# Kernel tuning notes

Hardware: AMD Instinct MI355X
Metric: run time of the kernel (lower is better)

The kernel has to match this reference:

```python
import jax, jax.numpy as jnp
import numpy as np

WINDOW = 60
DEPTH = 3
HIDDEN = 256
LN_EPS = 1e-5


def _lyndon_indices(d):
    # Lyndon words over alphabet {0..d-1}, lengths 2 and 3, lexicographic order
    # (signatory mode='words' extracts expanded-logsig coefficients at Lyndon words).
    i2 = np.array([(i, j) for i in range(d) for j in range(d) if (i, j) < (j, i)], dtype=np.int32)
    i3 = np.array([(i, j, k) for i in range(d) for j in range(d) for k in range(d)
                   if (i, j, k) < (j, k, i) and (i, j, k) < (k, i, j)], dtype=np.int32)
    return i2, i3


def _logsig_features(x):
    # x: [b, s, c] -> logsignature of time-augmented sliding windows: [b*s, sig_channels]
    b, s, c = x.shape
    d = c + 1
    # replicate-padded sliding windows via clipped gather (matches F.pad replicate + unfold)
    pos = jnp.clip(jnp.arange(s)[:, None] + jnp.arange(WINDOW)[None, :] - (WINDOW - 1), 0, s - 1)
    windows = x[:, pos, :]                                   # [b, s, W, c]
    t = jnp.linspace(0.0, 1.0, WINDOW, dtype=x.dtype)        # time augmentation channel
    t_b = jnp.broadcast_to(t[None, None, :, None], (b, s, WINDOW, 1))
    aug = jnp.concatenate([t_b, windows], axis=-1).reshape(b * s, WINDOW, d)
    N = b * s
    # basepoint=True: prepend zero point -> increments include the first point itself
    inc = jnp.diff(aug, axis=1, prepend=jnp.zeros((N, 1, d), aug.dtype))  # [N, W, d]
    inc_t = jnp.transpose(inc, (1, 0, 2))                    # [W, N, d]

    def chen_step(carry, v):
        S1, S2, S3 = carry
        vv = jnp.einsum('ni,nj->nij', v, v)
        vvv = jnp.einsum('nij,nk->nijk', vv, v)
        nS3 = S3 + jnp.einsum('nij,nk->nijk', S2, v) \
                 + 0.5 * jnp.einsum('ni,njk->nijk', S1, vv) + vvv / 6.0
        nS2 = S2 + jnp.einsum('ni,nj->nij', S1, v) + 0.5 * vv
        nS1 = S1 + v
        return (nS1, nS2, nS3), None

    init = (jnp.zeros((N, d), x.dtype), jnp.zeros((N, d, d), x.dtype), jnp.zeros((N, d, d, d), x.dtype))
    (S1, S2, S3), _ = jax.lax.scan(chen_step, init, inc_t)
    # log in truncated tensor algebra: log(1+x) = x - x^2/2 + x^3/3
    L1 = S1
    L2 = S2 - 0.5 * jnp.einsum('ni,nj->nij', S1, S1)
    L3 = (S3 - 0.5 * (jnp.einsum('ni,njk->nijk', S1, S2) + jnp.einsum('nij,nk->nijk', S2, S1))
          + jnp.einsum('ni,nj,nk->nijk', S1, S1, S1) / 3.0)
    i2, i3 = _lyndon_indices(d)
    f2 = L2[:, i2[:, 0], i2[:, 1]]
    f3 = L3[:, i3[:, 0], i3[:, 1], i3[:, 2]]
    return jnp.concatenate([L1, f2, f3], axis=-1)            # [N, sig_channels]


def setup_inputs() -> dict:
    key = jax.random.key(0)
    ks = jax.random.split(key, 5)
    b, s, c = 8, 2048, 8
    d = c + 1
    sig_channels = d + (d * d - d) // 2 + (d ** 3 - d) // 3  # 285 for d=9
    h2 = 2 * HIDDEN
    x = jax.random.normal(ks[0], (b, s, c), dtype=jnp.float32)
    w1 = jax.random.normal(ks[1], (sig_channels, h2), dtype=jnp.float32) / np.sqrt(sig_channels)
    b1 = jnp.zeros((h2,), jnp.float32)
    ln_g = jnp.ones((h2,), jnp.float32)
    ln_b = jnp.zeros((h2,), jnp.float32)
    w2 = jax.random.normal(ks[2], (h2, HIDDEN), dtype=jnp.float32) / np.sqrt(h2)
    b2 = jnp.zeros((HIDDEN,), jnp.float32)
    return {"x": x, "w1": w1, "b1": b1, "ln_g": ln_g, "ln_b": ln_b, "w2": w2, "b2": b2}


def reference(x, w1, b1, ln_g, ln_b, w2, b2):
    b, s, _ = x.shape
    feats = _logsig_features(x)                              # [b*s, sig_channels]
    h = jax.nn.gelu(feats @ w1 + b1, approximate=False)      # torch default GELU (erf)
    mu = jnp.mean(h, axis=-1, keepdims=True)
    var = jnp.var(h, axis=-1, keepdims=True)
    h = (h - mu) / jnp.sqrt(var + LN_EPS) * ln_g + ln_b      # LayerNorm; Dropout is eval no-op
    out = h @ w2 + b2
    return out.reshape(b, s, -1)
```

## Files before the change

### kernel.cpp

```cpp
#include <hip/hip_runtime.h>
#include <hip/hip_bf16.h>
#include <cstdint>
#include <cstddef>

typedef short short8 __attribute__((ext_vector_type(8)));
typedef float f32x4 __attribute__((ext_vector_type(4)));
typedef float f32x2 __attribute__((ext_vector_type(2)));

#define NS    2048
#define KPAD  288
#define H2    512
#define HID   256
#define WPB   7
#define SBLK  293

#define MFMA(a,b,c) __builtin_amdgcn_mfma_f32_16x16x32_bf16((a),(b),(c),0,0,0)

__device__ __forceinline__ void gl2lds16(const void* g, void* l) {
    __builtin_amdgcn_global_load_lds(
        (const __attribute__((address_space(1))) void*)g,
        (__attribute__((address_space(3))) void*)l, 16, 0, 0);
}
__device__ __forceinline__ float geluf(float x) {
    return 0.5f * x * (1.0f + erff(x * 0.70710678118654752f));
}
__device__ __forceinline__ f32x4 shfl4(f32x4 v, int d) {
    f32x4 r;
    r[0] = __shfl_xor(v[0], d); r[1] = __shfl_xor(v[1], d);
    r[2] = __shfl_xor(v[2], d); r[3] = __shfl_xor(v[3], d);
    return r;
}

struct Tbl3 { short col[729]; };
static constexpr Tbl3 make_tbl3() {
    Tbl3 t{};
    for (int x = 0; x < 729; ++x) t.col[x] = -1;
    int r = 0;
    for (int i = 0; i < 9; ++i)
        for (int j = 0; j < 9; ++j)
            for (int k = 0; k < 9; ++k) {
                bool lt1 = (i < j) || (i == j && (j < k || (j == k && k < i)));
                bool lt2 = (i < k) || (i == k && (j < i || (j == i && k < j)));
                if (lt1 && lt2) { t.col[(i*9+j)*9+k] = (short)(45 + r); ++r; }
            }
    return t;
}
static constexpr Tbl3 TBL3 = make_tbl3();

#define SIG_STEP(VA_,VB_,VC_) { \
    const float hh = 0.5f * S1i + vi * (1.0f/6.0f); \
    const float ra = S2ra + hh * (VA_); \
    const float rb = S2rb + hh * (VB_); \
    const float rc = S2rc + hh * (VC_); \
    const f32x2 ra2 = {ra, ra}, rb2 = {rb, rb}, rc2 = {rc, rc}; \
    S3sa += ra * v0; S3pa0 += ra2*vp0; S3pa1 += ra2*vp1; S3pa2 += ra2*vp2; S3pa3 += ra2*vp3; \
    S3sb += rb * v0; S3pb0 += rb2*vp0; S3pb1 += rb2*vp1; S3pb2 += rb2*vp2; S3pb3 += rb2*vp3; \
    S3sc += rc * v0; S3pc0 += rc2*vp0; S3pc1 += rc2*vp1; S3pc2 += rc2*vp2; S3pc3 += rc2*vp3; \
    const float aa = S1i + 0.5f * vi; \
    S2ra += aa * (VA_); S2rb += aa * (VB_); S2rc += aa * (VC_); \
    S1i += vi; }

#define SIG_MAIN(VA_,VB_,VC_) { \
    { const float* xr = &X[(g0 - lo) * 8]; \
      const float4 e0 = *(const float4*)xr; \
      const float4 e1 = *(const float4*)(xr + 4); \
      const float rs = xr[ioff]; \
      const float v0 = 0.0f; \
      const f32x2 vp0 = {e0.x, e0.y}, vp1 = {e0.z, e0.w}, vp2 = {e1.x, e1.y}, vp3 = {e1.z, e1.w}; \
      const float vi = (ci == 0) ? 0.0f : rs; \
      SIG_STEP(VA_,VB_,VC_) } \
    const float* pd = &PD[(sm59 + 1 - lo + 59) * 8]; \
    float4 d0 = *(const float4*)pd; \
    float4 d1 = *(const float4*)(pd + 4); \
    float rn = pd[ioff]; \
    _Pragma("unroll 2") \
    for (int j = 1; j < 60; ++j) { \
      const float4 e0 = d0; const float4 e1 = d1; const float rs = rn; \
      pd += 8; \
      d0 = *(const float4*)pd; d1 = *(const float4*)(pd + 4); rn = pd[ioff]; \
      const float v0 = DT; \
      const f32x2 vp0 = {e0.x, e0.y}, vp1 = {e0.z, e0.w}, vp2 = {e1.x, e1.y}, vp3 = {e1.z, e1.w}; \
      const float vi = (ci == 0) ? DT : rs; \
      SIG_STEP(VA_,VB_,VC_) \
    } }

#define SIG_ST(RA,RB,RC) \
    if (act) { \
        if ((RA) == 0) S1buf[widx * 9 + ci] = S1i; \
        float* sb = &S2buf[widx * 81 + ci * 9]; \
        sb[RA] = S2ra; sb[RB] = S2rb; sb[RC] = S2rc; \
    }

#define S3EL0(SL) S3s##SL
#define S3EL1(SL) S3p##SL##0[0]
#define S3EL2(SL) S3p##SL##0[1]
#define S3EL3(SL) S3p##SL##1[0]
#define S3EL4(SL) S3p##SL##1[1]
#define S3EL5(SL) S3p##SL##2[0]
#define S3EL6(SL) S3p##SL##2[1]
#define S3EL7(SL) S3p##SL##3[0]
#define S3EL8(SL) S3p##SL##3[1]

#define SIG_E2(SL,J2) if (ci < (J2)) { \
    const float val2 = S2r##SL - 0.5f * S1i * s1v##J2; \
    const int col2 = 9 + ci*8 - (ci*(ci-1))/2 + ((J2) - ci - 1); \
    frow[col2] = __float2bfloat16(val2); }

#define SIG_E3(SL,R,K) { const int col3 = TBL3.col[tb + (R)*9 + (K)]; \
    if (col3 >= 0) { \
        const float val3 = S3EL##K(SL) \
            - 0.5f * (S1i * S2w[(R)*9+(K)] + S2r##SL * s1v##K) \
            + S1i * s1v##R * s1v##K * (1.0f/3.0f); \
        frow[col3] = __float2bfloat16(val3); } }

#define SIG_E3R(SL,R) SIG_E3(SL,R,0) SIG_E3(SL,R,1) SIG_E3(SL,R,2) SIG_E3(SL,R,3) \
    SIG_E3(SL,R,4) SIG_E3(SL,R,5) SIG_E3(SL,R,6) SIG_E3(SL,R,7) SIG_E3(SL,R,8)

#define SIG_EMIT(RA,RB,RC) \
    if (act) { \
        if ((RA) == 0) { \
            frow[ci] = __float2bfloat16(S1i); \
            if (ci == 0) { \
                const __hip_bfloat16 z16 = __float2bfloat16(0.0f); \
                frow[285] = z16; frow[286] = z16; frow[287] = z16; \
            } \
        } \
        SIG_E2(a,RA) SIG_E2(b,RB) SIG_E2(c,RC) \
        SIG_E3R(a,RA) SIG_E3R(b,RB) SIG_E3R(c,RC) \
    }

__global__ __launch_bounds__(192) __attribute__((amdgpu_waves_per_eu(1, 6)))
void sig_kernel(const float* __restrict__ x, __hip_bfloat16* __restrict__ feats) {
    __shared__ __align__(16) float X[66 * 8];
    __shared__ __align__(16) float PD[126 * 8];
    __shared__ float S2buf[WPB * 81];
    __shared__ float S1buf[WPB * 9];

    const int blk = blockIdx.x;
    const int b   = blk / SBLK;
    const int s0  = (blk % SBLK) * WPB;
    const int lo  = (s0 - 59 > 0) ? (s0 - 59) : 0;
    const int hi  = (s0 + WPB - 1 < NS - 1) ? (s0 + WPB - 1) : (NS - 1);
    const int nrow = hi - lo + 1;
    const int tid = threadIdx.x;

    {
        const float4* src = (const float4*)(x + ((size_t)b * NS + lo) * 8);
        float4* X4 = (float4*)X;
        const int n4 = nrow * 2;
        for (int t = tid; t < n4; t += 192) X4[t] = src[t];
    }
    __syncthreads();
    {
        const float4* X4 = (const float4*)X;
        float4* PD4 = (float4*)PD;
        for (int t = tid; t < 252; t += 192) {
            const int p = t >> 1;
            const int r = p - 59;
            float4 dv = {0.f, 0.f, 0.f, 0.f};
            if (r > 0 && r < nrow) {
                const float4 a = X4[t - 118], bb = X4[t - 120];
                dv.x = a.x - bb.x; dv.y = a.y - bb.y; dv.z = a.z - bb.z; dv.w = a.w - bb.w;
            }
            PD4[t] = dv;
        }
    }
    __syncthreads();

    const int t3    = tid >> 6;
    const int lt    = tid & 63;
    const int widx0 = lt / 9;
    const int ci    = lt - widx0 * 9;
    const bool act  = (lt < 63) && (s0 + widx0 < NS);
    const int widx  = (widx0 < WPB - 1) ? widx0 : WPB - 1;
    int s = s0 + widx; if (s > NS - 1) s = NS - 1;

    float S3sa=0.f, S3sb=0.f, S3sc=0.f;
    f32x2 S3pa0={0.f,0.f},S3pa1={0.f,0.f},S3pa2={0.f,0.f},S3pa3={0.f,0.f};
    f32x2 S3pb0={0.f,0.f},S3pb1={0.f,0.f},S3pb2={0.f,0.f},S3pb3={0.f,0.f};
    f32x2 S3pc0={0.f,0.f},S3pc1={0.f,0.f},S3pc2={0.f,0.f},S3pc3={0.f,0.f};
    float S2ra=0.f, S2rb=0.f, S2rc=0.f;
    float S1i = 0.f;
    const int ioff = (ci > 0) ? (ci - 1) : 0;
    const int sm59 = s - 59;
    const int g0   = (sm59 > 0) ? sm59 : 0;
    const float DT = 1.0f / 59.0f;

    if (t3 == 0)      { SIG_MAIN(v0,   e0.x, e0.y) }
    else if (t3 == 1) { SIG_MAIN(e0.z, e0.w, e1.x) }
    else              { SIG_MAIN(e1.y, e1.z, e1.w) }

    if (t3 == 0)      { SIG_ST(0,1,2) }
    else if (t3 == 1) { SIG_ST(3,4,5) }
    else              { SIG_ST(6,7,8) }
    __syncthreads();

    const float* s1p = &S1buf[widx * 9];
    const float s1v0=s1p[0], s1v1=s1p[1], s1v2=s1p[2], s1v3=s1p[3], s1v4=s1p[4];
    const float s1v5=s1p[5], s1v6=s1p[6], s1v7=s1p[7], s1v8=s1p[8];
    const float* S2w = &S2buf[widx * 81];
    const int tb = ci * 81;
    __hip_bfloat16* frow = feats + (size_t)(b * NS + s) * KPAD;

    if (t3 == 0)      { SIG_EMIT(0,1,2) }
    else if (t3 == 1) { SIG_EMIT(3,4,5) }
    else              { SIG_EMIT(6,7,8) }
}

__global__ __launch_bounds__(512)
void prep_kernel(const float* __restrict__ w1, const float* __restrict__ w2,
                 const float* __restrict__ lng, const float* __restrict__ lnb,
                 const float* __restrict__ b2,
                 __hip_bfloat16* __restrict__ w1T, __hip_bfloat16* __restrict__ w2g,
                 float* __restrict__ gw, float* __restrict__ cvec,
                 float* __restrict__ stats) {
    const int blk = blockIdx.x;
    if (blk < 256) {
        const int n = blk, k = threadIdx.x;
        const float wv = w2[(size_t)k * HID + n];
        const float a = lng[k] * wv;
        const float c = lnb[k] * wv;
        w2g[(size_t)n * H2 + k] = __float2bfloat16(a);
        float ra = a, rc = c;
#pragma unroll
        for (int d = 1; d < 64; d <<= 1) { ra += __shfl_xor(ra, d); rc += __shfl_xor(rc, d); }
        __shared__ float r1[8], r2[8];
        const int wv_ = k >> 6, ln = k & 63;
        if (ln == 0) { r1[wv_] = ra; r2[wv_] = rc; }
        __syncthreads();
        if (k == 0) {
            float sa = 0.f, sc = 0.f;
#pragma unroll
            for (int i = 0; i < 8; ++i) { sa += r1[i]; sc += r2[i]; }
            gw[n] = sa; cvec[n] = sc + b2[n];
        }
    } else {
        const int n = blk - 256;
        const int k = threadIdx.x;
        if (k < KPAD) {
            const float v = (k < 285) ? w1[(size_t)k * H2 + n] : 0.0f;
            w1T[(size_t)n * KPAD + k] = __float2bfloat16(v);
        }
        if (k < 64) stats[n * 64 + k] = 0.0f;
    }
}

#define GDECL \
    f32x4 acc00={0,0,0,0},acc01={0,0,0,0},acc02={0,0,0,0},acc03={0,0,0,0}; \
    f32x4 acc10={0,0,0,0},acc11={0,0,0,0},acc12={0,0,0,0},acc13={0,0,0,0}; \
    f32x4 acc20={0,0,0,0},acc21={0,0,0,0},acc22={0,0,0,0},acc23={0,0,0,0}; \
    f32x4 acc30={0,0,0,0},acc31={0,0,0,0},acc32={0,0,0,0},acc33={0,0,0,0};

#define GMROW(mf) { const short8 av = *(const short8*)(abase + (mf)*512); \
    acc##mf##0 = MFMA(av, b0v, acc##mf##0); acc##mf##1 = MFMA(av, b1v, acc##mf##1); \
    acc##mf##2 = MFMA(av, b2v, acc##mf##2); acc##mf##3 = MFMA(av, b3v, acc##mf##3); }

#define GSTAGE(APTR, BPTR, KD, K0, LA, LB) { \
    int c = tid; \
    gl2lds16((APTR) + (size_t)(m0 + (c>>2))*(KD) + (K0) + (c&3)*8, (char*)(LA) + (c & ~63)*16); \
    gl2lds16((BPTR) + (size_t)(n0 + (c>>2))*(KD) + (K0) + (c&3)*8, (char*)(LB) + (c & ~63)*16); \
    c = tid + 256; \
    gl2lds16((APTR) + (size_t)(m0 + (c>>2))*(KD) + (K0) + (c&3)*8, (char*)(LA) + (c & ~63)*16); \
    gl2lds16((BPTR) + (size_t)(n0 + (c>>2))*(KD) + (K0) + (c&3)*8, (char*)(LB) + (c & ~63)*16); }

#define GCOMP(LA, LB) { \
    const __hip_bfloat16* abase = (LA) + (mh + l16)*32 + quad*8; \
    const __hip_bfloat16* bbase = (LB) + (nh + l16)*32 + quad*8; \
    const short8 b0v = *(const short8*)(bbase); \
    const short8 b1v = *(const short8*)(bbase + 512); \
    const short8 b2v = *(const short8*)(bbase + 1024); \
    const short8 b3v = *(const short8*)(bbase + 1536); \
    GMROW(0) GMROW(1) GMROW(2) GMROW(3) }

#define GEMM_PIPE(APTR, BPTR, KD, KSTEPS) \
    GSTAGE(APTR, BPTR, KD, 0, ldsA0, ldsB0) \
    __syncthreads(); \
    _Pragma("unroll 1") \
    for (int kt = 0; kt < (KSTEPS); kt += 2) { \
        if (kt + 1 < (KSTEPS)) { GSTAGE(APTR, BPTR, KD, (kt+1)*32, ldsA1, ldsB1) } \
        GCOMP(ldsA0, ldsB0) \
        __syncthreads(); \
        if (kt + 1 < (KSTEPS)) { \
            if (kt + 2 < (KSTEPS)) { GSTAGE(APTR, BPTR, KD, (kt+2)*32, ldsA0, ldsB0) } \
            GCOMP(ldsA1, ldsB1) \
            __syncthreads(); \
        } \
    }

#define G1EP(mf,nf) { \
    const int colv = n0 + nh + (nf)*16 + l16; \
    const float bv = bias[colv]; \
    f32x4 e; \
    e[0] = geluf(acc##mf##nf[0] + bv); e[1] = geluf(acc##mf##nf[1] + bv); \
    e[2] = geluf(acc##mf##nf[2] + bv); e[3] = geluf(acc##mf##nf[3] + bv); \
    const int rrow = m0 + mh + (mf)*16 + quad*4; \
    h1[(size_t)(rrow+0)*H2 + colv] = __float2bfloat16(e[0]); \
    h1[(size_t)(rrow+1)*H2 + colv] = __float2bfloat16(e[1]); \
    h1[(size_t)(rrow+2)*H2 + colv] = __float2bfloat16(e[2]); \
    h1[(size_t)(rrow+3)*H2 + colv] = __float2bfloat16(e[3]); \
    sum##mf += e; sq##mf += e*e; }

#define G1RED(mf) { \
    f32x4 s = sum##mf, q = sq##mf; \
    s += shfl4(s,1); q += shfl4(q,1); s += shfl4(s,2); q += shfl4(q,2); \
    s += shfl4(s,4); q += shfl4(q,4); s += shfl4(s,8); q += shfl4(q,8); \
    if (l16 == 0) { const int rrow = m0 + mh + (mf)*16 + quad*4; \
        atomicAdd(&stats[2*(rrow+0)],   s[0]); atomicAdd(&stats[2*(rrow+0)+1], q[0]); \
        atomicAdd(&stats[2*(rrow+1)],   s[1]); atomicAdd(&stats[2*(rrow+1)+1], q[1]); \
        atomicAdd(&stats[2*(rrow+2)],   s[2]); atomicAdd(&stats[2*(rrow+2)+1], q[2]); \
        atomicAdd(&stats[2*(rrow+3)],   s[3]); atomicAdd(&stats[2*(rrow+3)+1], q[3]); } }

__global__ __launch_bounds__(256) __attribute__((amdgpu_waves_per_eu(1, 4)))
void gemm1_kernel(const __hip_bfloat16* __restrict__ feats,
                  const __hip_bfloat16* __restrict__ w1T,
                  const float* __restrict__ bias,
                  __hip_bfloat16* __restrict__ h1,
                  float* __restrict__ stats) {
    __shared__ __align__(16) __hip_bfloat16 ldsA0[128 * 32];
    __shared__ __align__(16) __hip_bfloat16 ldsB0[128 * 32];
    __shared__ __align__(16) __hip_bfloat16 ldsA1[128 * 32];
    __shared__ __align__(16) __hip_bfloat16 ldsB1[128 * 32];
    const int tid  = threadIdx.x;
    const int wave = tid >> 6;
    const int lane = tid & 63;
    const int quad = lane >> 4;
    const int l16  = lane & 15;
    const int mh   = (wave >> 1) * 64;
    const int nh   = (wave & 1) * 64;
    const int m0   = blockIdx.x * 128;
    const int n0   = blockIdx.y * 128;
    GDECL
    GEMM_PIPE(feats, w1T, KPAD, 9)
    f32x4 sum0={0,0,0,0},sum1={0,0,0,0},sum2={0,0,0,0},sum3={0,0,0,0};
    f32x4 sq0={0,0,0,0},sq1={0,0,0,0},sq2={0,0,0,0},sq3={0,0,0,0};
    G1EP(0,0) G1EP(0,1) G1EP(0,2) G1EP(0,3)
    G1EP(1,0) G1EP(1,1) G1EP(1,2) G1EP(1,3)
    G1EP(2,0) G1EP(2,1) G1EP(2,2) G1EP(2,3)
    G1EP(3,0) G1EP(3,1) G1EP(3,2) G1EP(3,3)
    G1RED(0) G1RED(1) G1RED(2) G1RED(3)
}

#define STATR(r) { const float su = stats[2*(rrow+(r))]; const float qu = stats[2*(rrow+(r))+1]; \
    const float m_ = su * (1.0f/512.0f); const float v_ = qu * (1.0f/512.0f) - m_*m_; \
    muv[r] = m_; rsv[r] = rsqrtf(v_ + 1e-5f); }

#define G2C(mf,nf) { const int colv = n0 + nh + (nf)*16 + l16; \
    const float g_ = gw[colv], c_ = cvec[colv]; \
    out[(size_t)(rrow+0)*HID + colv] = rsv[0]*(acc##mf##nf[0] - muv[0]*g_) + c_; \
    out[(size_t)(rrow+1)*HID + colv] = rsv[1]*(acc##mf##nf[1] - muv[1]*g_) + c_; \
    out[(size_t)(rrow+2)*HID + colv] = rsv[2]*(acc##mf##nf[2] - muv[2]*g_) + c_; \
    out[(size_t)(rrow+3)*HID + colv] = rsv[3]*(acc##mf##nf[3] - muv[3]*g_) + c_; }

#define G2EP(mf) { const int rrow = m0 + mh + (mf)*16 + quad*4; \
    f32x4 muv, rsv; \
    STATR(0) STATR(1) STATR(2) STATR(3) \
    G2C(mf,0) G2C(mf,1) G2C(mf,2) G2C(mf,3) }

__global__ __launch_bounds__(256) __attribute__((amdgpu_waves_per_eu(1, 4)))
void gemm2_kernel(const __hip_bfloat16* __restrict__ h1,
                  const __hip_bfloat16* __restrict__ w2g,
                  const float* __restrict__ stats,
                  const float* __restrict__ gw,
                  const float* __restrict__ cvec,
                  float* __restrict__ out) {
    __shared__ __align__(16) __hip_bfloat16 ldsA0[128 * 32];
    __shared__ __align__(16) __hip_bfloat16 ldsB0[128 * 32];
    __shared__ __align__(16) __hip_bfloat16 ldsA1[128 * 32];
    __shared__ __align__(16) __hip_bfloat16 ldsB1[128 * 32];
    const int tid  = threadIdx.x;
    const int wave = tid >> 6;
    const int lane = tid & 63;
    const int quad = lane >> 4;
    const int l16  = lane & 15;
    const int mh   = (wave >> 1) * 64;
    const int nh   = (wave & 1) * 64;
    const int m0   = blockIdx.x * 128;
    const int n0   = blockIdx.y * 128;
    GDECL
    GEMM_PIPE(h1, w2g, H2, 16)
    G2EP(0) G2EP(1) G2EP(2) G2EP(3)
}

extern "C" void kernel_launch(void* const* d_in, const int* in_sizes, int n_in,
                              void* d_out, int out_size, void* d_ws, size_t ws_size,
                              hipStream_t stream) {
    const float* x   = (const float*)d_in[0];
    const float* w1  = (const float*)d_in[1];
    const float* b1  = (const float*)d_in[2];
    const float* lng = (const float*)d_in[3];
    const float* lnb = (const float*)d_in[4];
    const float* w2  = (const float*)d_in[5];
    const float* b2  = (const float*)d_in[6];
    float* out = (float*)d_out;

    char* ws = (char*)d_ws;
    __hip_bfloat16* feats = (__hip_bfloat16*)(ws);
    __hip_bfloat16* h1    = (__hip_bfloat16*)(ws + 9437184);
    __hip_bfloat16* w1T   = (__hip_bfloat16*)(ws + 26214400);
    __hip_bfloat16* w2g   = (__hip_bfloat16*)(ws + 26509312);
    float*          gw    = (float*)(ws + 26771456);
    float*          cvec  = (float*)(ws + 26775552);
    float*          stats = (float*)(ws + 26779648);

    prep_kernel<<<dim3(768), dim3(512), 0, stream>>>(w1, w2, lng, lnb, b2,
                                                     w1T, w2g, gw, cvec, stats);
    sig_kernel<<<dim3(8 * SBLK), dim3(192), 0, stream>>>(x, feats);
    gemm1_kernel<<<dim3(128, 4), dim3(256), 0, stream>>>(feats, w1T, b1, h1, stats);
    gemm2_kernel<<<dim3(128, 2), dim3(256), 0, stream>>>(h1, w2g, stats, gw, cvec, out);
}
```

Baseline: 155.5 us.

## Fuse both MLP GEMMs and LayerNorm into one kernel keeping hidden activations in LDS

Replaces the separate gemm1 and gemm2 kernels with a single mlp_kernel in which each block owns 32 rows. GEMM1 computes all 512 hidden columns per row, applies GELU, and writes the bf16 result into a swizzled LDS buffer. LayerNorm row statistics are reduced in shared memory instead of through global atomics. GEMM2 then reads the hidden tile straight from LDS. This removes the h1 round trip through global memory, one kernel launch, and the atomic stats buffer, but every block now streams the full W1 and W2 weights with a small 32-row M tile and uses a large LDS footprint, which limits occupancy.

```diff
diff --git a/kernel.cpp b/kernel.cpp
--- a/kernel.cpp
+++ b/kernel.cpp
@@ -212,8 +212,7 @@
                  const float* __restrict__ lng, const float* __restrict__ lnb,
                  const float* __restrict__ b2,
                  __hip_bfloat16* __restrict__ w1T, __hip_bfloat16* __restrict__ w2g,
-                 float* __restrict__ gw, float* __restrict__ cvec,
-                 float* __restrict__ stats) {
+                 float* __restrict__ gw, float* __restrict__ cvec) {
     const int blk = blockIdx.x;
     if (blk < 256) {
         const int n = blk, k = threadIdx.x;
@@ -241,144 +240,165 @@
             const float v = (k < 285) ? w1[(size_t)k * H2 + n] : 0.0f;
             w1T[(size_t)n * KPAD + k] = __float2bfloat16(v);
         }
-        if (k < 64) stats[n * 64 + k] = 0.0f;
-    }
-}
-
-#define GDECL \
-    f32x4 acc00={0,0,0,0},acc01={0,0,0,0},acc02={0,0,0,0},acc03={0,0,0,0}; \
-    f32x4 acc10={0,0,0,0},acc11={0,0,0,0},acc12={0,0,0,0},acc13={0,0,0,0}; \
-    f32x4 acc20={0,0,0,0},acc21={0,0,0,0},acc22={0,0,0,0},acc23={0,0,0,0}; \
-    f32x4 acc30={0,0,0,0},acc31={0,0,0,0},acc32={0,0,0,0},acc33={0,0,0,0};
-
-#define GMROW(mf) { const short8 av = *(const short8*)(abase + (mf)*512); \
-    acc##mf##0 = MFMA(av, b0v, acc##mf##0); acc##mf##1 = MFMA(av, b1v, acc##mf##1); \
-    acc##mf##2 = MFMA(av, b2v, acc##mf##2); acc##mf##3 = MFMA(av, b3v, acc##mf##3); }
-
-#define GSTAGE(APTR, BPTR, KD, K0, LA, LB) { \
-    int c = tid; \
-    gl2lds16((APTR) + (size_t)(m0 + (c>>2))*(KD) + (K0) + (c&3)*8, (char*)(LA) + (c & ~63)*16); \
-    gl2lds16((BPTR) + (size_t)(n0 + (c>>2))*(KD) + (K0) + (c&3)*8, (char*)(LB) + (c & ~63)*16); \
-    c = tid + 256; \
-    gl2lds16((APTR) + (size_t)(m0 + (c>>2))*(KD) + (K0) + (c&3)*8, (char*)(LA) + (c & ~63)*16); \
-    gl2lds16((BPTR) + (size_t)(n0 + (c>>2))*(KD) + (K0) + (c&3)*8, (char*)(LB) + (c & ~63)*16); }
-
-#define GCOMP(LA, LB) { \
-    const __hip_bfloat16* abase = (LA) + (mh + l16)*32 + quad*8; \
-    const __hip_bfloat16* bbase = (LB) + (nh + l16)*32 + quad*8; \
-    const short8 b0v = *(const short8*)(bbase); \
-    const short8 b1v = *(const short8*)(bbase + 512); \
-    const short8 b2v = *(const short8*)(bbase + 1024); \
-    const short8 b3v = *(const short8*)(bbase + 1536); \
-    GMROW(0) GMROW(1) GMROW(2) GMROW(3) }
-
-#define GEMM_PIPE(APTR, BPTR, KD, KSTEPS) \
-    GSTAGE(APTR, BPTR, KD, 0, ldsA0, ldsB0) \
-    __syncthreads(); \
-    _Pragma("unroll 1") \
-    for (int kt = 0; kt < (KSTEPS); kt += 2) { \
-        if (kt + 1 < (KSTEPS)) { GSTAGE(APTR, BPTR, KD, (kt+1)*32, ldsA1, ldsB1) } \
-        GCOMP(ldsA0, ldsB0) \
-        __syncthreads(); \
-        if (kt + 1 < (KSTEPS)) { \
-            if (kt + 2 < (KSTEPS)) { GSTAGE(APTR, BPTR, KD, (kt+2)*32, ldsA0, ldsB0) } \
-            GCOMP(ldsA1, ldsB1) \
-            __syncthreads(); \
-        } \
-    }
-
-#define G1EP(mf,nf) { \
-    const int colv = n0 + nh + (nf)*16 + l16; \
-    const float bv = bias[colv]; \
-    f32x4 e; \
-    e[0] = geluf(acc##mf##nf[0] + bv); e[1] = geluf(acc##mf##nf[1] + bv); \
-    e[2] = geluf(acc##mf##nf[2] + bv); e[3] = geluf(acc##mf##nf[3] + bv); \
-    const int rrow = m0 + mh + (mf)*16 + quad*4; \
-    h1[(size_t)(rrow+0)*H2 + colv] = __float2bfloat16(e[0]); \
-    h1[(size_t)(rrow+1)*H2 + colv] = __float2bfloat16(e[1]); \
-    h1[(size_t)(rrow+2)*H2 + colv] = __float2bfloat16(e[2]); \
-    h1[(size_t)(rrow+3)*H2 + colv] = __float2bfloat16(e[3]); \
-    sum##mf += e; sq##mf += e*e; }
-
-#define G1RED(mf) { \
-    f32x4 s = sum##mf, q = sq##mf; \
-    s += shfl4(s,1); q += shfl4(q,1); s += shfl4(s,2); q += shfl4(q,2); \
-    s += shfl4(s,4); q += shfl4(q,4); s += shfl4(s,8); q += shfl4(q,8); \
-    if (l16 == 0) { const int rrow = m0 + mh + (mf)*16 + quad*4; \
-        atomicAdd(&stats[2*(rrow+0)],   s[0]); atomicAdd(&stats[2*(rrow+0)+1], q[0]); \
-        atomicAdd(&stats[2*(rrow+1)],   s[1]); atomicAdd(&stats[2*(rrow+1)+1], q[1]); \
-        atomicAdd(&stats[2*(rrow+2)],   s[2]); atomicAdd(&stats[2*(rrow+2)+1], q[2]); \
-        atomicAdd(&stats[2*(rrow+3)],   s[3]); atomicAdd(&stats[2*(rrow+3)+1], q[3]); } }
-
-__global__ __launch_bounds__(256) __attribute__((amdgpu_waves_per_eu(1, 4)))
-void gemm1_kernel(const __hip_bfloat16* __restrict__ feats,
-                  const __hip_bfloat16* __restrict__ w1T,
-                  const float* __restrict__ bias,
-                  __hip_bfloat16* __restrict__ h1,
-                  float* __restrict__ stats) {
-    __shared__ __align__(16) __hip_bfloat16 ldsA0[128 * 32];
-    __shared__ __align__(16) __hip_bfloat16 ldsB0[128 * 32];
-    __shared__ __align__(16) __hip_bfloat16 ldsA1[128 * 32];
-    __shared__ __align__(16) __hip_bfloat16 ldsB1[128 * 32];
+    }
+}
+
+__global__ __launch_bounds__(256)
+void mlp_kernel(const __hip_bfloat16* __restrict__ feats,
+                const __hip_bfloat16* __restrict__ w1T,
+                const float* __restrict__ bias,
+                const __hip_bfloat16* __restrict__ w2g,
+                const float* __restrict__ gw,
+                const float* __restrict__ cvec,
+                float* __restrict__ out) {
+    __shared__ __align__(16) __hip_bfloat16 Blds[512 * 32];
+    __shared__ __align__(16) __hip_bfloat16 Hbuf[32 * 512];
+    __shared__ __align__(16) __hip_bfloat16 Ab0[32 * 32];
+    __shared__ __align__(16) __hip_bfloat16 Ab1[32 * 32];
+    __shared__ float sstat[4][32][2];
+
     const int tid  = threadIdx.x;
     const int wave = tid >> 6;
     const int lane = tid & 63;
     const int quad = lane >> 4;
     const int l16  = lane & 15;
-    const int mh   = (wave >> 1) * 64;
-    const int nh   = (wave & 1) * 64;
-    const int m0   = blockIdx.x * 128;
-    const int n0   = blockIdx.y * 128;
-    GDECL
-    GEMM_PIPE(feats, w1T, KPAD, 9)
-    f32x4 sum0={0,0,0,0},sum1={0,0,0,0},sum2={0,0,0,0},sum3={0,0,0,0};
-    f32x4 sq0={0,0,0,0},sq1={0,0,0,0},sq2={0,0,0,0},sq3={0,0,0,0};
-    G1EP(0,0) G1EP(0,1) G1EP(0,2) G1EP(0,3)
-    G1EP(1,0) G1EP(1,1) G1EP(1,2) G1EP(1,3)
-    G1EP(2,0) G1EP(2,1) G1EP(2,2) G1EP(2,3)
-    G1EP(3,0) G1EP(3,1) G1EP(3,2) G1EP(3,3)
-    G1RED(0) G1RED(1) G1RED(2) G1RED(3)
-}
-
-#define STATR(r) { const float su = stats[2*(rrow+(r))]; const float qu = stats[2*(rrow+(r))+1]; \
-    const float m_ = su * (1.0f/512.0f); const float v_ = qu * (1.0f/512.0f) - m_*m_; \
-    muv[r] = m_; rsv[r] = rsqrtf(v_ + 1e-5f); }
-
-#define G2C(mf,nf) { const int colv = n0 + nh + (nf)*16 + l16; \
-    const float g_ = gw[colv], c_ = cvec[colv]; \
-    out[(size_t)(rrow+0)*HID + colv] = rsv[0]*(acc##mf##nf[0] - muv[0]*g_) + c_; \
-    out[(size_t)(rrow+1)*HID + colv] = rsv[1]*(acc##mf##nf[1] - muv[1]*g_) + c_; \
-    out[(size_t)(rrow+2)*HID + colv] = rsv[2]*(acc##mf##nf[2] - muv[2]*g_) + c_; \
-    out[(size_t)(rrow+3)*HID + colv] = rsv[3]*(acc##mf##nf[3] - muv[3]*g_) + c_; }
-
-#define G2EP(mf) { const int rrow = m0 + mh + (mf)*16 + quad*4; \
-    f32x4 muv, rsv; \
-    STATR(0) STATR(1) STATR(2) STATR(3) \
-    G2C(mf,0) G2C(mf,1) G2C(mf,2) G2C(mf,3) }
-
-__global__ __launch_bounds__(256) __attribute__((amdgpu_waves_per_eu(1, 4)))
-void gemm2_kernel(const __hip_bfloat16* __restrict__ h1,
-                  const __hip_bfloat16* __restrict__ w2g,
-                  const float* __restrict__ stats,
-                  const float* __restrict__ gw,
-                  const float* __restrict__ cvec,
-                  float* __restrict__ out) {
-    __shared__ __align__(16) __hip_bfloat16 ldsA0[128 * 32];
-    __shared__ __align__(16) __hip_bfloat16 ldsB0[128 * 32];
-    __shared__ __align__(16) __hip_bfloat16 ldsA1[128 * 32];
-    __shared__ __align__(16) __hip_bfloat16 ldsB1[128 * 32];
-    const int tid  = threadIdx.x;
-    const int wave = tid >> 6;
-    const int lane = tid & 63;
-    const int quad = lane >> 4;
-    const int l16  = lane & 15;
-    const int mh   = (wave >> 1) * 64;
-    const int nh   = (wave & 1) * 64;
-    const int m0   = blockIdx.x * 128;
-    const int n0   = blockIdx.y * 128;
-    GDECL
-    GEMM_PIPE(h1, w2g, H2, 16)
-    G2EP(0) G2EP(1) G2EP(2) G2EP(3)
+    const int m0   = blockIdx.x * 32;
+    const int swz16 = (quad ^ ((l16 >> 1) & 3)) * 16;
+
+#define STAGE_B1(S, DST) { \
+    _Pragma("unroll") \
+    for (int i_ = 0; i_ < 8; ++i_) { \
+        const int c_ = tid + i_ * 256; const int r_ = c_ >> 2; const int q_ = c_ & 3; \
+        gl2lds16(w1T + (size_t)r_ * KPAD + (S) * 32 + ((q_ ^ ((r_ >> 1) & 3)) * 8), \
+                 (char*)(DST) + (c_ & ~63) * 16); } }
+#define STAGE_A(S, DST) { if (tid < 128) { \
+        const int r_ = tid >> 2; const int q_ = tid & 3; \
+        gl2lds16(feats + (size_t)(m0 + r_) * KPAD + (S) * 32 + ((q_ ^ ((r_ >> 1) & 3)) * 8), \
+                 (char*)(DST) + (tid & ~63) * 16); } }
+#define STAGE_B2(T, DST) { \
+    _Pragma("unroll") \
+    for (int i_ = 0; i_ < 4; ++i_) { \
+        const int c_ = tid + i_ * 256; const int r_ = c_ >> 2; const int q_ = c_ & 3; \
+        gl2lds16(w2g + (size_t)r_ * H2 + (T) * 32 + ((q_ ^ ((r_ >> 1) & 3)) * 8), \
+                 (char*)(DST) + (c_ & ~63) * 16); } }
+
+    ((float*)sstat)[tid] = 0.0f;
+    STAGE_B1(0, Blds)
+    STAGE_A(0, Ab0)
+    __syncthreads();
+
+    f32x4 a1[2][8];
+#pragma unroll
+    for (int mf = 0; mf < 2; ++mf)
+#pragma unroll
+        for (int nf = 0; nf < 8; ++nf) a1[mf][nf] = f32x4{0.f, 0.f, 0.f, 0.f};
+
+#pragma unroll 1
+    for (int s = 0; s < 9; ++s) {
+        if (s < 8) {
+            if ((s + 1) & 1) { STAGE_B1(s + 1, Hbuf) STAGE_A(s + 1, Ab1) }
+            else             { STAGE_B1(s + 1, Blds) STAGE_A(s + 1, Ab0) }
+        }
+        const char* Ac = (s & 1) ? (const char*)Ab1 : (const char*)Ab0;
+        const char* Bc = (s & 1) ? (const char*)Hbuf : (const char*)Blds;
+        const short8 av0 = *(const short8*)(Ac + l16 * 64 + swz16);
+        const short8 av1 = *(const short8*)(Ac + (16 + l16) * 64 + swz16);
+#pragma unroll
+        for (int nf = 0; nf < 8; ++nf) {
+            const short8 bv = *(const short8*)(Bc + (size_t)(wave * 128 + nf * 16 + l16) * 64 + swz16);
+            a1[0][nf] = MFMA(av0, bv, a1[0][nf]);
+            a1[1][nf] = MFMA(av1, bv, a1[1][nf]);
+        }
+        __syncthreads();
+    }
+
+    {
+        f32x4 sum0 = {0,0,0,0}, sum1 = {0,0,0,0}, sq0 = {0,0,0,0}, sq1 = {0,0,0,0};
+#pragma unroll
+        for (int nf = 0; nf < 8; ++nf) {
+            const int col = wave * 128 + nf * 16 + l16;
+            const float bv = bias[col];
+            f32x4 e0, e1;
+#pragma unroll
+            for (int r = 0; r < 4; ++r) { e0[r] = geluf(a1[0][nf][r] + bv); e1[r] = geluf(a1[1][nf][r] + bv); }
+#pragma unroll
+            for (int r = 0; r < 4; ++r) {
+                const int row0 = quad * 4 + r;
+                const int row1 = 16 + row0;
+                const int ch0 = (col >> 3) ^ (row0 & 7);
+                const int ch1 = (col >> 3) ^ (row1 & 7);
+                *(__hip_bfloat16*)((char*)Hbuf + row0 * 1024 + ch0 * 16 + (col & 7) * 2) = __float2bfloat16(e0[r]);
+                *(__hip_bfloat16*)((char*)Hbuf + row1 * 1024 + ch1 * 16 + (col & 7) * 2) = __float2bfloat16(e1[r]);
+            }
+            sum0 += e0; sq0 += e0 * e0; sum1 += e1; sq1 += e1 * e1;
+        }
+        sum0 += shfl4(sum0, 1); sq0 += shfl4(sq0, 1); sum1 += shfl4(sum1, 1); sq1 += shfl4(sq1, 1);
+        sum0 += shfl4(sum0, 2); sq0 += shfl4(sq0, 2); sum1 += shfl4(sum1, 2); sq1 += shfl4(sq1, 2);
+        sum0 += shfl4(sum0, 4); sq0 += shfl4(sq0, 4); sum1 += shfl4(sum1, 4); sq1 += shfl4(sq1, 4);
+        sum0 += shfl4(sum0, 8); sq0 += shfl4(sq0, 8); sum1 += shfl4(sum1, 8); sq1 += shfl4(sq1, 8);
+        if (l16 == 0) {
+#pragma unroll
+            for (int r = 0; r < 4; ++r) {
+                sstat[wave][quad * 4 + r][0]      = sum0[r];
+                sstat[wave][quad * 4 + r][1]      = sq0[r];
+                sstat[wave][16 + quad * 4 + r][0] = sum1[r];
+                sstat[wave][16 + quad * 4 + r][1] = sq1[r];
+            }
+        }
+        __syncthreads();
+    }
+
+    f32x4 a2[2][4];
+#pragma unroll
+    for (int mf = 0; mf < 2; ++mf)
+#pragma unroll
+        for (int nf = 0; nf < 4; ++nf) a2[mf][nf] = f32x4{0.f, 0.f, 0.f, 0.f};
+
+    STAGE_B2(0, Blds)
+    __syncthreads();
+
+    const int hsw = l16 & 7;
+#pragma unroll 1
+    for (int t = 0; t < 16; ++t) {
+        if (t < 15) { STAGE_B2(t + 1, (char*)Blds + ((t + 1) & 1) * 16384) }
+        const char* Bc = (const char*)Blds + (t & 1) * 16384;
+        const int kc = ((t * 4 + quad) ^ hsw) * 16;
+        const short8 hv0 = *(const short8*)((const char*)Hbuf + l16 * 1024 + kc);
+        const short8 hv1 = *(const short8*)((const char*)Hbuf + (16 + l16) * 1024 + kc);
+#pragma unroll
+        for (int nf = 0; nf < 4; ++nf) {
+            const short8 bv = *(const short8*)(Bc + (size_t)(wave * 64 + nf * 16 + l16) * 64 + swz16);
+            a2[0][nf] = MFMA(hv0, bv, a2[0][nf]);
+            a2[1][nf] = MFMA(hv1, bv, a2[1][nf]);
+        }
+        __syncthreads();
+    }
+
+    f32x4 mu0, rs0, mu1, rs1;
+#pragma unroll
+    for (int r = 0; r < 4; ++r) {
+        const int rl0 = quad * 4 + r, rl1 = 16 + rl0;
+        const float s0 = sstat[0][rl0][0] + sstat[1][rl0][0] + sstat[2][rl0][0] + sstat[3][rl0][0];
+        const float q0 = sstat[0][rl0][1] + sstat[1][rl0][1] + sstat[2][rl0][1] + sstat[3][rl0][1];
+        const float s1 = sstat[0][rl1][0] + sstat[1][rl1][0] + sstat[2][rl1][0] + sstat[3][rl1][0];
+        const float q1 = sstat[0][rl1][1] + sstat[1][rl1][1] + sstat[2][rl1][1] + sstat[3][rl1][1];
+        mu0[r] = s0 * (1.0f / 512.0f);
+        mu1[r] = s1 * (1.0f / 512.0f);
+        rs0[r] = rsqrtf(q0 * (1.0f / 512.0f) - mu0[r] * mu0[r] + 1e-5f);
+        rs1[r] = rsqrtf(q1 * (1.0f / 512.0f) - mu1[r] * mu1[r] + 1e-5f);
+    }
+#pragma unroll
+    for (int nf = 0; nf < 4; ++nf) {
+        const int col = wave * 64 + nf * 16 + l16;
+        const float g_ = gw[col], c_ = cvec[col];
+#pragma unroll
+        for (int r = 0; r < 4; ++r) {
+            const int row0 = m0 + quad * 4 + r;
+            const int row1 = row0 + 16;
+            out[(size_t)row0 * HID + col] = rs0[r] * (a2[0][nf][r] - mu0[r] * g_) + c_;
+            out[(size_t)row1 * HID + col] = rs1[r] * (a2[1][nf][r] - mu1[r] * g_) + c_;
+        }
+    }
 }
 
 extern "C" void kernel_launch(void* const* d_in, const int* in_sizes, int n_in,
@@ -395,16 +415,13 @@
 
     char* ws = (char*)d_ws;
     __hip_bfloat16* feats = (__hip_bfloat16*)(ws);
-    __hip_bfloat16* h1    = (__hip_bfloat16*)(ws + 9437184);
-    __hip_bfloat16* w1T   = (__hip_bfloat16*)(ws + 26214400);
-    __hip_bfloat16* w2g   = (__hip_bfloat16*)(ws + 26509312);
-    float*          gw    = (float*)(ws + 26771456);
-    float*          cvec  = (float*)(ws + 26775552);
-    float*          stats = (float*)(ws + 26779648);
+    __hip_bfloat16* w1T   = (__hip_bfloat16*)(ws + 9437184);
+    __hip_bfloat16* w2g   = (__hip_bfloat16*)(ws + 9732096);
+    float*          gw    = (float*)(ws + 9994240);
+    float*          cvec  = (float*)(ws + 9995264);
 
     prep_kernel<<<dim3(768), dim3(512), 0, stream>>>(w1, w2, lng, lnb, b2,
-                                                     w1T, w2g, gw, cvec, stats);
+                                                     w1T, w2g, gw, cvec);
     sig_kernel<<<dim3(8 * SBLK), dim3(192), 0, stream>>>(x, feats);
-    gemm1_kernel<<<dim3(128, 4), dim3(256), 0, stream>>>(feats, w1T, b1, h1, stats);
-    gemm2_kernel<<<dim3(128, 2), dim3(256), 0, stream>>>(h1, w2g, stats, gw, cvec, out);
-}
+    mlp_kernel<<<dim3(512), dim3(256), 0, stream>>>(feats, w1T, b1, w2g, gw, cvec, out);
+}
```

New measurement: 149.8 us. 1.04x faster.
